# Optimization experiments

Hardware: AMD Instinct MI355X
Metric: run time of the kernel (lower is better)

Reference implementation:

```python
import jax, jax.numpy as jnp
import numpy as np

EMBED_DIM = 768
NUM_HEADS = 12
HEAD_DIM = EMBED_DIM // NUM_HEADS
SCALE = HEAD_DIM ** -0.5


def setup_inputs() -> dict:
    key = jax.random.key(0)
    ks = jax.random.split(key, 5)
    B, T, D = 8, 1024, EMBED_DIM
    lim_qkv = (1.0 / D) ** 0.5
    x = jax.random.normal(ks[0], (B, T, D), dtype=jnp.float32)
    W_qkv = jax.random.uniform(ks[1], (D, 3 * D), dtype=jnp.float32, minval=-lim_qkv, maxval=lim_qkv)
    b_qkv = jax.random.uniform(ks[2], (3 * D,), dtype=jnp.float32, minval=-lim_qkv, maxval=lim_qkv)
    W_proj = jax.random.uniform(ks[3], (D, D), dtype=jnp.float32, minval=-lim_qkv, maxval=lim_qkv)
    b_proj = jax.random.uniform(ks[4], (D,), dtype=jnp.float32, minval=-lim_qkv, maxval=lim_qkv)
    return {"x": x, "W_qkv": W_qkv, "b_qkv": b_qkv, "W_proj": W_proj, "b_proj": b_proj}


def reference(x, W_qkv, b_qkv, W_proj, b_proj):
    B, T, D = x.shape
    H, Hd = NUM_HEADS, HEAD_DIM
    # fused QKV projection: [B,T,3D] -> [3,B,H,T,Hd]
    qkv = (x @ W_qkv + b_qkv).reshape(B, T, 3, H, Hd).transpose(2, 0, 3, 1, 4)
    q, k, v = qkv[0], qkv[1], qkv[2]
    attn = jax.nn.softmax(jnp.einsum("bhqd,bhkd->bhqk", q, k) * SCALE, axis=-1)
    out = jnp.einsum("bhqk,bhkd->bhqd", attn, v)  # [B,H,T,Hd]
    out = out.transpose(0, 2, 1, 3).reshape(B, T, D)
    return out @ W_proj + b_proj
```

## Files before the change

### kernel.cpp

```cpp
#include <hip/hip_runtime.h>
#include <hip/hip_bf16.h>
#include <stdint.h>

#define NB 8
#define NT 1024
#define ND 768
#define NH 12

static constexpr float QSCALE = 0.125f * 1.44269504f;

typedef __bf16 bf16x8 __attribute__((ext_vector_type(8)));
typedef float f32x4 __attribute__((ext_vector_type(4)));
typedef unsigned short u16;

__device__ __forceinline__ u16 f2b(float f) {
  union { float f; uint32_t u; } c; c.f = f;
  uint32_t u = c.u;
  u += 0x7fffu + ((u >> 16) & 1u);
  return (u16)(u >> 16);
}

__device__ __forceinline__ uint32_t pk2(float a, float b) {
  __hip_bfloat162 p = __float22bfloat162_rn(make_float2(a, b));
  return *reinterpret_cast<uint32_t*>(&p);
}

__device__ __forceinline__ float exp2_raw(float x) {
  float y;
  asm("v_exp_f32 %0, %1" : "=v"(y) : "v"(x));
  return y;
}

__device__ __forceinline__ void gload16(const void* g, void* l) {
  __builtin_amdgcn_global_load_lds(
      (const __attribute__((address_space(1))) void*)g,
      (__attribute__((address_space(3))) void*)l, 16, 0, 0);
}

__global__ void k_cast(const float* __restrict__ in, u16* __restrict__ out, int n4) {
  int i = blockIdx.x * blockDim.x + threadIdx.x;
  if (i >= n4) return;
  float4 v = reinterpret_cast<const float4*>(in)[i];
  ushort4 o;
  o.x = f2b(v.x); o.y = f2b(v.y); o.z = f2b(v.z); o.w = f2b(v.w);
  reinterpret_cast<ushort4*>(out)[i] = o;
}

__global__ void k_tcast(const float* __restrict__ in, u16* __restrict__ out, int R, int C) {
  __shared__ float tile[32][33];
  int c0 = blockIdx.x * 32, r0 = blockIdx.y * 32;
  int tx = threadIdx.x & 31, ty = threadIdx.x >> 5;
  #pragma unroll
  for (int rr = ty; rr < 32; rr += 8)
    tile[rr][tx] = in[(size_t)(r0 + rr) * C + c0 + tx];
  __syncthreads();
  #pragma unroll
  for (int cc = ty; cc < 32; cc += 8)
    out[(size_t)(c0 + cc) * R + r0 + tx] = f2b(tile[tx][cc]);
}

__launch_bounds__(256, 4)
__global__ void k_gemm_qkv(const u16* __restrict__ A, const u16* __restrict__ Bt,
                           const float* __restrict__ bias,
                           u16* __restrict__ Qg, u16* __restrict__ KV)
{
  __shared__ u16 Al[128 * 64];
  __shared__ u16 Bl[128 * 64];
  const int tid = threadIdx.x, lane = tid & 63, wv = tid >> 6;
  const int g = lane >> 4, r = lane & 15;
  const int wm = (wv >> 1) * 64, wn = (wv & 1) * 64;
  const int bid = blockIdx.x + blockIdx.y * 18;
  const int swz = (bid & 7) * 144 + (bid >> 3);
  const int m0 = (swz / 18) * 128, n0 = (swz % 18) * 128;
  const int srow = lane >> 3;
  const int scolsw = ((lane & 7) ^ (lane >> 3)) * 8;
  f32x4 acc[4][4] = {};
  for (int k0 = 0; k0 < ND; k0 += 64) {
    __syncthreads();
    #pragma unroll
    for (int i = 0; i < 4; ++i) {
      int c = wv * 4 + i;
      gload16(&A[(size_t)(m0 + c * 8 + srow) * ND + k0 + scolsw], &Al[c * 512]);
      gload16(&Bt[(size_t)(n0 + c * 8 + srow) * ND + k0 + scolsw], &Bl[c * 512]);
    }
    __syncthreads();
    #pragma unroll
    for (int kk = 0; kk < 2; ++kk) {
      bf16x8 af[4], bfr[4];
      #pragma unroll
      for (int mf = 0; mf < 4; ++mf)
        af[mf] = *reinterpret_cast<const bf16x8*>(
            &Al[(wm + mf * 16 + r) * 64 + (((kk << 2) + g) ^ (r & 7)) * 8]);
      #pragma unroll
      for (int nf = 0; nf < 4; ++nf)
        bfr[nf] = *reinterpret_cast<const bf16x8*>(
            &Bl[(wn + nf * 16 + r) * 64 + (((kk << 2) + g) ^ (r & 7)) * 8]);
      #pragma unroll
      for (int mf = 0; mf < 4; ++mf)
        #pragma unroll
        for (int nf = 0; nf < 4; ++nf)
          acc[mf][nf] = __builtin_amdgcn_mfma_f32_16x16x32_bf16(af[mf], bfr[nf], acc[mf][nf], 0, 0, 0);
    }
  }
  #pragma unroll
  for (int mf = 0; mf < 4; ++mf)
    #pragma unroll
    for (int nf = 0; nf < 4; ++nf) {
      int col = n0 + wn + nf * 16 + r;
      int which = col / ND, c = col - which * ND;
      int h = c >> 6, hd = c & 63;
      int row0 = m0 + wm + mf * 16 + 4 * g;
      int bb = row0 >> 10, t0 = row0 & 1023;
      size_t bh = (size_t)bb * NH + h;
      float b = bias[col];
      if (which == 0) {
        #pragma unroll
        for (int jj = 0; jj < 4; ++jj)
          Qg[(bh * NT + t0 + jj) * 64 + hd] = f2b((acc[mf][nf][jj] + b) * QSCALE);
      } else if (which == 1) {
        int kt = t0 >> 6, nfk = (t0 >> 4) & 3, rk0 = t0 & 15;
        int kk = hd >> 5, ghd = (hd >> 3) & 3, e = hd & 7;
        size_t base = (bh * 16 + kt) * 8192 + (size_t)(nfk * 2 + kk) * 512 + e;
        #pragma unroll
        for (int jj = 0; jj < 4; ++jj)
          KV[base + (ghd * 16 + rk0 + jj) * 8] = f2b(acc[mf][nf][jj] + b);
      } else {
        int kt = t0 >> 6, tl0 = t0 & 63;
        int ks = tl0 >> 5, gv = (tl0 >> 3) & 3, e0 = tl0 & 7;
        int hf = hd >> 4, rv = hd & 15;
        size_t base = (bh * 16 + kt) * 8192 + 4096 +
                      (size_t)(hf * 2 + ks) * 512 + (gv * 16 + rv) * 8 + e0;
        ushort4 o;
        o.x = f2b(acc[mf][nf][0] + b);
        o.y = f2b(acc[mf][nf][1] + b);
        o.z = f2b(acc[mf][nf][2] + b);
        o.w = f2b(acc[mf][nf][3] + b);
        *reinterpret_cast<ushort4*>(&KV[base]) = o;
      }
    }
}

__launch_bounds__(256, 4)
__global__ void k_attn(const u16* __restrict__ Qg, const u16* __restrict__ KV,
                       u16* __restrict__ Ob)
{
  __shared__ u16 Pl[4][1024];
  const int tid = threadIdx.x, lane = tid & 63, wv = tid >> 6;
  const int g = lane >> 4, r = lane & 15;
  const int bh = blockIdx.x;
  const int qt = blockIdx.y;
  const int bb = bh / NH, h = bh - bb * NH;
  const u16* Qb = Qg + (size_t)bh * NT * 64;
  const u16* kvb = KV + (size_t)bh * 16 * 8192;

  bf16x8 qf[2][2];
  #pragma unroll
  for (int mf = 0; mf < 2; ++mf)
    #pragma unroll
    for (int kk = 0; kk < 2; ++kk) {
      int qrow = qt * 128 + wv * 32 + mf * 16 + r;
      qf[mf][kk] = *reinterpret_cast<const bf16x8*>(&Qb[(size_t)qrow * 64 + kk * 32 + g * 8]);
    }

  bf16x8 ones;
  #pragma unroll
  for (int i = 0; i < 8; ++i) ones[i] = (__bf16)1.0f;

  f32x4 lacc[2] = {};
  f32x4 oacc[2][4] = {};
  u16* Pw = Pl[wv];

  for (int kt = 0; kt < 16; ++kt) {
    const u16* Kt = kvb + (size_t)kt * 8192;
    const u16* Vt = Kt + 4096;

    f32x4 st[2][4] = {};
    bf16x8 kf[4][2];
    #pragma unroll
    for (int nf = 0; nf < 4; ++nf)
      #pragma unroll
      for (int kk = 0; kk < 2; ++kk)
        kf[nf][kk] = *reinterpret_cast<const bf16x8*>(&Kt[(nf * 2 + kk) * 512 + lane * 8]);
    __builtin_amdgcn_s_setprio(1);
    #pragma unroll
    for (int kk = 0; kk < 2; ++kk)
      #pragma unroll
      for (int mf = 0; mf < 2; ++mf)
        #pragma unroll
        for (int nf = 0; nf < 4; ++nf)
          st[mf][nf] = __builtin_amdgcn_mfma_f32_16x16x32_bf16(kf[nf][kk], qf[mf][kk], st[mf][nf], 0, 0, 0);
    __builtin_amdgcn_s_setprio(0);

    #pragma unroll
    for (int mf = 0; mf < 2; ++mf)
      #pragma unroll
      for (int nf = 0; nf < 4; ++nf)
        #pragma unroll
        for (int jj = 0; jj < 4; ++jj)
          st[mf][nf][jj] = exp2_raw(st[mf][nf][jj]);

    #pragma unroll
    for (int ks = 0; ks < 2; ++ks) {
      #pragma unroll
      for (int mf = 0; mf < 2; ++mf)
        #pragma unroll
        for (int u = 0; u < 2; ++u) {
          uint2 w;
          w.x = pk2(st[mf][2 * ks + u][0], st[mf][2 * ks + u][1]);
          w.y = pk2(st[mf][2 * ks + u][2], st[mf][2 * ks + u][3]);
          int gp = u * 2 + (g >> 1);
          *reinterpret_cast<uint2*>(&Pw[mf * 512 + (gp * 16 + r) * 8 + (g & 1) * 4]) = w;
        }
      bf16x8 pf[2], vf[4];
      #pragma unroll
      for (int mf = 0; mf < 2; ++mf)
        pf[mf] = *reinterpret_cast<const bf16x8*>(&Pw[mf * 512 + lane * 8]);
      #pragma unroll
      for (int hf = 0; hf < 4; ++hf)
        vf[hf] = *reinterpret_cast<const bf16x8*>(&Vt[(hf * 2 + ks) * 512 + lane * 8]);
      __builtin_amdgcn_s_setprio(1);
      #pragma unroll
      for (int mf = 0; mf < 2; ++mf) {
        #pragma unroll
        for (int hf = 0; hf < 4; ++hf)
          oacc[mf][hf] = __builtin_amdgcn_mfma_f32_16x16x32_bf16(vf[hf], pf[mf], oacc[mf][hf], 0, 0, 0);
        lacc[mf] = __builtin_amdgcn_mfma_f32_16x16x32_bf16(ones, pf[mf], lacc[mf], 0, 0, 0);
      }
      __builtin_amdgcn_s_setprio(0);
    }
  }

  #pragma unroll
  for (int mf = 0; mf < 2; ++mf) {
    float inv = 1.f / lacc[mf][0];
    int row = qt * 128 + wv * 32 + mf * 16 + r;
    #pragma unroll
    for (int hf = 0; hf < 4; ++hf) {
      uint2 w;
      w.x = pk2(oacc[mf][hf][0] * inv, oacc[mf][hf][1] * inv);
      w.y = pk2(oacc[mf][hf][2] * inv, oacc[mf][hf][3] * inv);
      *reinterpret_cast<uint2*>(&Ob[((size_t)(bb * NT + row)) * ND + h * 64 + hf * 16 + 4 * g]) = w;
    }
  }
}

__launch_bounds__(256, 4)
__global__ void k_gemm_proj(const u16* __restrict__ A, const u16* __restrict__ Bt,
                            const float* __restrict__ bias, float* __restrict__ out)
{
  __shared__ u16 Al[128 * 32];
  __shared__ u16 Bl[64 * 32];
  const int tid = threadIdx.x, lane = tid & 63, wv = tid >> 6;
  const int g = lane >> 4, r = lane & 15;
  const int wm = (wv >> 1) * 64, wn = (wv & 1) * 32;
  const int bid = blockIdx.x + blockIdx.y * 12;
  const int swz = (bid & 7) * 96 + (bid >> 3);
  const int m0 = (swz / 12) * 128, n0 = (swz % 12) * 64;
  const int srow = lane >> 2;
  const int scol = (lane & 3) * 8;
  f32x4 acc[4][2] = {};
  for (int k0 = 0; k0 < ND; k0 += 32) {
    __syncthreads();
    #pragma unroll
    for (int i = 0; i < 2; ++i) {
      int c = wv * 2 + i;
      gload16(&A[(size_t)(m0 + c * 16 + srow) * ND + k0 + scol], &Al[c * 512]);
    }
    gload16(&Bt[(size_t)(n0 + wv * 16 + srow) * ND + k0 + scol], &Bl[wv * 512]);
    __syncthreads();
    bf16x8 af[4], bfr[2];
    #pragma unroll
    for (int mf = 0; mf < 4; ++mf)
      af[mf] = *reinterpret_cast<const bf16x8*>(&Al[(wm + mf * 16 + r) * 32 + g * 8]);
    #pragma unroll
    for (int nf = 0; nf < 2; ++nf)
      bfr[nf] = *reinterpret_cast<const bf16x8*>(&Bl[(wn + nf * 16 + r) * 32 + g * 8]);
    #pragma unroll
    for (int mf = 0; mf < 4; ++mf)
      #pragma unroll
      for (int nf = 0; nf < 2; ++nf)
        acc[mf][nf] = __builtin_amdgcn_mfma_f32_16x16x32_bf16(af[mf], bfr[nf], acc[mf][nf], 0, 0, 0);
  }
  #pragma unroll
  for (int mf = 0; mf < 4; ++mf)
    #pragma unroll
    for (int nf = 0; nf < 2; ++nf) {
      int col = n0 + wn + nf * 16 + r;
      float b = bias[col];
      #pragma unroll
      for (int jj = 0; jj < 4; ++jj) {
        int row = m0 + wm + mf * 16 + 4 * g + jj;
        out[(size_t)row * ND + col] = acc[mf][nf][jj] + b;
      }
    }
}

extern "C" void kernel_launch(void* const* d_in, const int* in_sizes, int n_in,
                              void* d_out, int out_size, void* d_ws, size_t ws_size,
                              hipStream_t stream)
{
  const float* x     = (const float*)d_in[0];
  const float* Wqkv  = (const float*)d_in[1];
  const float* bqkv  = (const float*)d_in[2];
  const float* Wproj = (const float*)d_in[3];
  const float* bproj = (const float*)d_in[4];
  float* out = (float*)d_out;

  char* ws = (char*)d_ws;
  u16* xb  = (u16*)(ws + 0);
  u16* wqt = (u16*)(ws + 12582912);
  u16* wpt = (u16*)(ws + 16121856);
  u16* Qg  = (u16*)(ws + 17301504);
  u16* KV  = (u16*)(ws + 29884416);
  u16* Ob  = (u16*)(ws + 55050240);

  k_cast<<<dim3((8192 * 768 / 4 + 255) / 256), dim3(256), 0, stream>>>(x, xb, 8192 * 768 / 4);
  k_tcast<<<dim3(2304 / 32, 768 / 32), dim3(256), 0, stream>>>(Wqkv, wqt, 768, 2304);
  k_tcast<<<dim3(768 / 32, 768 / 32), dim3(256), 0, stream>>>(Wproj, wpt, 768, 768);
  k_gemm_qkv<<<dim3(2304 / 128, 8192 / 128), dim3(256), 0, stream>>>(xb, wqt, bqkv, Qg, KV);
  k_attn<<<dim3(96, 8), dim3(256), 0, stream>>>(Qg, KV, Ob);
  k_gemm_proj<<<dim3(768 / 64, 8192 / 128), dim3(256), 0, stream>>>(Ob, wpt, bproj, out);
}
```

Before: 110.0 us.

## Double-buffer QKV GEMM LDS tiles and widen proj GEMM K-tile with swizzle

The QKV GEMM now uses two LDS buffers per operand and prefetches the tile two steps ahead, with explicit vmcnt waits and raw barriers so global loads overlap MFMA work. It also raises wave priority around the MFMA block. The projection GEMM doubles its K-step to 64 and uses the XOR-swizzled LDS layout, halving loop iterations and barriers while reducing bank conflicts. In exchange, QKV LDS use doubles and its launch bound occupancy hint drops to 2 blocks per SIMD group, which may reduce concurrency.

```diff
diff --git a/kernel.cpp b/kernel.cpp
--- a/kernel.cpp
+++ b/kernel.cpp
@@ -59,13 +59,13 @@
     out[(size_t)(c0 + cc) * R + r0 + tx] = f2b(tile[tx][cc]);
 }
 
-__launch_bounds__(256, 4)
+__launch_bounds__(256, 2)
 __global__ void k_gemm_qkv(const u16* __restrict__ A, const u16* __restrict__ Bt,
                            const float* __restrict__ bias,
                            u16* __restrict__ Qg, u16* __restrict__ KV)
 {
-  __shared__ u16 Al[128 * 64];
-  __shared__ u16 Bl[128 * 64];
+  __shared__ u16 Al[2][8192];
+  __shared__ u16 Bl[2][8192];
   const int tid = threadIdx.x, lane = tid & 63, wv = tid >> 6;
   const int g = lane >> 4, r = lane & 15;
   const int wm = (wv >> 1) * 64, wn = (wv & 1) * 64;
@@ -74,34 +74,56 @@
   const int m0 = (swz / 18) * 128, n0 = (swz % 18) * 128;
   const int srow = lane >> 3;
   const int scolsw = ((lane & 7) ^ (lane >> 3)) * 8;
+
+  #define STG(k0, ab)                                                                     \
+    do {                                                                                  \
+      _Pragma("unroll")                                                                   \
+      for (int i = 0; i < 4; ++i) {                                                       \
+        int c = wv * 4 + i;                                                               \
+        gload16(&A[(size_t)(m0 + c * 8 + srow) * ND + (k0) + scolsw], &Al[ab][c * 512]);  \
+        gload16(&Bt[(size_t)(n0 + c * 8 + srow) * ND + (k0) + scolsw], &Bl[ab][c * 512]); \
+      }                                                                                   \
+    } while (0)
+
   f32x4 acc[4][4] = {};
-  for (int k0 = 0; k0 < ND; k0 += 64) {
-    __syncthreads();
-    #pragma unroll
-    for (int i = 0; i < 4; ++i) {
-      int c = wv * 4 + i;
-      gload16(&A[(size_t)(m0 + c * 8 + srow) * ND + k0 + scolsw], &Al[c * 512]);
-      gload16(&Bt[(size_t)(n0 + c * 8 + srow) * ND + k0 + scolsw], &Bl[c * 512]);
-    }
-    __syncthreads();
+  STG(0, 0);
+  STG(64, 1);
+  asm volatile("s_waitcnt vmcnt(8)" ::: "memory");
+  __builtin_amdgcn_s_barrier();
+
+  for (int t = 0; t < 12; ++t) {
+    const int kb = t & 1;
     #pragma unroll
     for (int kk = 0; kk < 2; ++kk) {
       bf16x8 af[4], bfr[4];
       #pragma unroll
       for (int mf = 0; mf < 4; ++mf)
         af[mf] = *reinterpret_cast<const bf16x8*>(
-            &Al[(wm + mf * 16 + r) * 64 + (((kk << 2) + g) ^ (r & 7)) * 8]);
+            &Al[kb][(wm + mf * 16 + r) * 64 + (((kk << 2) + g) ^ (r & 7)) * 8]);
       #pragma unroll
       for (int nf = 0; nf < 4; ++nf)
         bfr[nf] = *reinterpret_cast<const bf16x8*>(
-            &Bl[(wn + nf * 16 + r) * 64 + (((kk << 2) + g) ^ (r & 7)) * 8]);
+            &Bl[kb][(wn + nf * 16 + r) * 64 + (((kk << 2) + g) ^ (r & 7)) * 8]);
+      __builtin_amdgcn_s_setprio(1);
       #pragma unroll
       for (int mf = 0; mf < 4; ++mf)
         #pragma unroll
         for (int nf = 0; nf < 4; ++nf)
           acc[mf][nf] = __builtin_amdgcn_mfma_f32_16x16x32_bf16(af[mf], bfr[nf], acc[mf][nf], 0, 0, 0);
-    }
+      __builtin_amdgcn_s_setprio(0);
+    }
+    asm volatile("s_waitcnt lgkmcnt(0)" ::: "memory");
+    __builtin_amdgcn_s_barrier();
+    if (t <= 9) {
+      STG((t + 2) * 64, kb);
+      asm volatile("s_waitcnt vmcnt(8)" ::: "memory");
+    } else {
+      asm volatile("s_waitcnt vmcnt(0)" ::: "memory");
+    }
+    __builtin_amdgcn_s_barrier();
   }
+  #undef STG
+
   #pragma unroll
   for (int mf = 0; mf < 4; ++mf)
     #pragma unroll
@@ -248,38 +270,45 @@
 __global__ void k_gemm_proj(const u16* __restrict__ A, const u16* __restrict__ Bt,
                             const float* __restrict__ bias, float* __restrict__ out)
 {
-  __shared__ u16 Al[128 * 32];
-  __shared__ u16 Bl[64 * 32];
+  __shared__ u16 Al[128 * 64];
+  __shared__ u16 Bl[64 * 64];
   const int tid = threadIdx.x, lane = tid & 63, wv = tid >> 6;
   const int g = lane >> 4, r = lane & 15;
   const int wm = (wv >> 1) * 64, wn = (wv & 1) * 32;
   const int bid = blockIdx.x + blockIdx.y * 12;
   const int swz = (bid & 7) * 96 + (bid >> 3);
   const int m0 = (swz / 12) * 128, n0 = (swz % 12) * 64;
-  const int srow = lane >> 2;
-  const int scol = (lane & 3) * 8;
+  const int srow = lane >> 3;
+  const int scolsw = ((lane & 7) ^ (lane >> 3)) * 8;
   f32x4 acc[4][2] = {};
-  for (int k0 = 0; k0 < ND; k0 += 32) {
+  for (int k0 = 0; k0 < ND; k0 += 64) {
     __syncthreads();
     #pragma unroll
-    for (int i = 0; i < 2; ++i) {
-      int c = wv * 2 + i;
-      gload16(&A[(size_t)(m0 + c * 16 + srow) * ND + k0 + scol], &Al[c * 512]);
-    }
-    gload16(&Bt[(size_t)(n0 + wv * 16 + srow) * ND + k0 + scol], &Bl[wv * 512]);
+    for (int i = 0; i < 6; ++i) {
+      int c = wv * 6 + i;
+      if (c < 16)
+        gload16(&A[(size_t)(m0 + c * 8 + srow) * ND + k0 + scolsw], &Al[c * 512]);
+      else
+        gload16(&Bt[(size_t)(n0 + (c - 16) * 8 + srow) * ND + k0 + scolsw], &Bl[(c - 16) * 512]);
+    }
     __syncthreads();
-    bf16x8 af[4], bfr[2];
-    #pragma unroll
-    for (int mf = 0; mf < 4; ++mf)
-      af[mf] = *reinterpret_cast<const bf16x8*>(&Al[(wm + mf * 16 + r) * 32 + g * 8]);
-    #pragma unroll
-    for (int nf = 0; nf < 2; ++nf)
-      bfr[nf] = *reinterpret_cast<const bf16x8*>(&Bl[(wn + nf * 16 + r) * 32 + g * 8]);
-    #pragma unroll
-    for (int mf = 0; mf < 4; ++mf)
+    #pragma unroll
+    for (int kk = 0; kk < 2; ++kk) {
+      bf16x8 af[4], bfr[2];
+      #pragma unroll
+      for (int mf = 0; mf < 4; ++mf)
+        af[mf] = *reinterpret_cast<const bf16x8*>(
+            &Al[(wm + mf * 16 + r) * 64 + (((kk << 2) + g) ^ (r & 7)) * 8]);
       #pragma unroll
       for (int nf = 0; nf < 2; ++nf)
-        acc[mf][nf] = __builtin_amdgcn_mfma_f32_16x16x32_bf16(af[mf], bfr[nf], acc[mf][nf], 0, 0, 0);
+        bfr[nf] = *reinterpret_cast<const bf16x8*>(
+            &Bl[(wn + nf * 16 + r) * 64 + (((kk << 2) + g) ^ (r & 7)) * 8]);
+      #pragma unroll
+      for (int mf = 0; mf < 4; ++mf)
+        #pragma unroll
+        for (int nf = 0; nf < 2; ++nf)
+          acc[mf][nf] = __builtin_amdgcn_mfma_f32_16x16x32_bf16(af[mf], bfr[nf], acc[mf][nf], 0, 0, 0);
+    }
   }
   #pragma unroll
   for (int mf = 0; mf < 4; ++mf)
```

Result: slower. 112.2 us (+2.0%).
